# Optimization experiments

Hardware: AMD Instinct MI355X
Metric: run time of the kernel (lower is better)

Reference implementation:

```python
import jax, jax.numpy as jnp
import numpy as np

EMB = 768
N_HEADS = 12
HEAD_DIM = EMB // N_HEADS
EPS = 1e-5


def _gelu_tanh(x):
    c = jnp.sqrt(jnp.asarray(2.0 / jnp.pi, x.dtype))
    return 0.5 * x * (1.0 + jnp.tanh(c * (x + 0.044715 * x ** 3)))


def _layernorm(x, scale, shift):
    mean = jnp.mean(x, axis=-1, keepdims=True)
    var = jnp.mean((x - mean) ** 2, axis=-1, keepdims=True)
    return (x - mean) / jnp.sqrt(var + EPS) * scale + shift


def setup_inputs() -> dict:
    key = jax.random.key(0)
    ks = jax.random.split(key, 8)
    s = 0.02  # GPT-2 style init scale
    x = jax.random.normal(ks[0], (8, 1024, EMB), dtype=jnp.float32)
    # torch Linear weights are (out, in); no biases (qkv_bias=False everywhere)
    wq = jax.random.normal(ks[1], (EMB, EMB), dtype=jnp.float32) * s
    wk = jax.random.normal(ks[2], (EMB, EMB), dtype=jnp.float32) * s
    wv = jax.random.normal(ks[3], (EMB, EMB), dtype=jnp.float32) * s
    wo = jax.random.normal(ks[4], (EMB, EMB), dtype=jnp.float32) * s
    w1 = jax.random.normal(ks[5], (4 * EMB, EMB), dtype=jnp.float32) * s
    w2 = jax.random.normal(ks[6], (EMB, 4 * EMB), dtype=jnp.float32) * s
    ln1_scale = jnp.ones((EMB,), jnp.float32)
    ln1_shift = jnp.zeros((EMB,), jnp.float32)
    ln2_scale = jnp.ones((EMB,), jnp.float32)
    ln2_shift = jnp.zeros((EMB,), jnp.float32)
    return dict(x=x, wq=wq, wk=wk, wv=wv, wo=wo, w1=w1, w2=w2,
                ln1_scale=ln1_scale, ln1_shift=ln1_shift,
                ln2_scale=ln2_scale, ln2_shift=ln2_shift)


def reference(x, wq, wk, wv, wo, w1, w2, ln1_scale, ln1_shift, ln2_scale, ln2_shift):
    B, T, E = x.shape
    # --- attention sublayer (pre-LN) ---
    h = _layernorm(x, ln1_scale, ln1_shift)
    q = (h @ wq.T).reshape(B, T, N_HEADS, HEAD_DIM).transpose(0, 2, 1, 3)
    k = (h @ wk.T).reshape(B, T, N_HEADS, HEAD_DIM).transpose(0, 2, 1, 3)
    v = (h @ wv.T).reshape(B, T, N_HEADS, HEAD_DIM).transpose(0, 2, 1, 3)
    scores = jnp.einsum('bhqd,bhkd->bhqk', q, k)  # [B,H,T,T]
    causal = jnp.tril(jnp.ones((T, T), dtype=bool))
    scores = jnp.where(causal, scores, -jnp.inf)
    attn = jax.nn.softmax(scores / np.sqrt(HEAD_DIM), axis=-1)
    ctx = jnp.einsum('bhqk,bhkd->bhqd', attn, v)
    ctx = ctx.transpose(0, 2, 1, 3).reshape(B, T, E)
    x = x + ctx @ wo.T
    # --- FFN sublayer (pre-LN) ---
    h = _layernorm(x, ln2_scale, ln2_shift)
    h = _gelu_tanh(h @ w1.T) @ w2.T
    return x + h
```

## Files before the change

kernel.cpp:

```cpp
#include <hip/hip_runtime.h>
#include <hip/hip_bf16.h>
#include <cstdint>

#define EMB    768
#define NHEADS 12
#define HDIM   64
#define SEQ    1024
#define BATCH  8
#define MROWS  (BATCH*SEQ)
#define FFN    3072
#define W2E    (EMB*EMB)
#define W4E    (FFN*EMB)

typedef __bf16 bf16_t;
typedef bf16_t bf16x8 __attribute__((ext_vector_type(8)));
typedef float  f32x4  __attribute__((ext_vector_type(4)));

__device__ __forceinline__ float b2f(unsigned short u) {
    union { unsigned int i; float f; } t; t.i = ((unsigned int)u) << 16; return t.f;
}
__device__ __forceinline__ unsigned short f2b(float f) {
    union { float f; unsigned int i; } t; t.f = f;
    unsigned int lsb = (t.i >> 16) & 1u;
    t.i += 0x7fffu + lsb;
    return (unsigned short)(t.i >> 16);
}

#if defined(__has_builtin)
#if __has_builtin(__builtin_amdgcn_global_load_lds)
#define HAS_GLL 1
#endif
#endif
#ifndef HAS_GLL
#define HAS_GLL 0
#endif

__device__ __forceinline__ void gll16(const unsigned short* g, unsigned short* lds_wave_base) {
#if HAS_GLL
    __builtin_amdgcn_global_load_lds(
        (const __attribute__((address_space(1))) unsigned int*)g,
        (__attribute__((address_space(3))) unsigned int*)lds_wave_base, 16, 0, 0);
#endif
}

__device__ __forceinline__ int4 load8(const void* src, size_t eoff, bool f32) {
    if (f32) {
        const float4* p = reinterpret_cast<const float4*>((const float*)src + eoff);
        float4 a = p[0], b = p[1];
        union { unsigned short u[8]; int4 v; } r;
        r.u[0] = f2b(a.x); r.u[1] = f2b(a.y); r.u[2] = f2b(a.z); r.u[3] = f2b(a.w);
        r.u[4] = f2b(b.x); r.u[5] = f2b(b.y); r.u[6] = f2b(b.z); r.u[7] = f2b(b.w);
        return r.v;
    }
    return *reinterpret_cast<const int4*>((const unsigned short*)src + eoff);
}
__device__ __forceinline__ float4 load4f(const void* src, size_t eoff, bool f32) {
    if (f32) return *reinterpret_cast<const float4*>((const float*)src + eoff);
    ushort4 u = *reinterpret_cast<const ushort4*>((const unsigned short*)src + eoff);
    float4 r; r.x = b2f(u.x); r.y = b2f(u.y); r.z = b2f(u.z); r.w = b2f(u.w);
    return r;
}

struct DetectArgs { const unsigned short* p[11]; int n[11]; };

__global__ __launch_bounds__(256) void detect_all(DetectArgs a, int* __restrict__ flags) {
    __shared__ int cnt;
    if (threadIdx.x == 0) cnt = 0;
    __syncthreads();
    const unsigned short* src = a.p[blockIdx.x];
    int npairs = a.n[blockIdx.x] / 2;
    if (npairs > 4096) npairs = 4096;
    int local = 0;
    for (int p = threadIdx.x; p < npairs; p += 256) {
        unsigned short u0 = src[2 * p], u1 = src[2 * p + 1];
        int e0 = (u0 >> 7) & 0xFF;
        bool insane0 = (e0 == 0xFF) || (u0 != 0 && (e0 < 96 || e0 > 159));
        bool zpat    = (u0 == 0 && u1 != 0);
        if (insane0 || zpat) ++local;
    }
    atomicAdd(&cnt, local);
    __syncthreads();
    if (threadIdx.x == 0) flags[blockIdx.x] = (cnt * 8 > npairs) ? 1 : 0;
}

__global__ __launch_bounds__(256) void cvt_adapt(
        const void* __restrict__ src, unsigned short* __restrict__ dst,
        int n, const int* __restrict__ flag) {
    int i = blockIdx.x * 256 + threadIdx.x;
    if (i * 4 >= n) return;
    if (*flag) {
        float4 f = reinterpret_cast<const float4*>(src)[i];
        ushort4 o;
        o.x = f2b(f.x); o.y = f2b(f.y); o.z = f2b(f.z); o.w = f2b(f.w);
        reinterpret_cast<ushort4*>(dst)[i] = o;
    } else {
        reinterpret_cast<ushort4*>(dst)[i] = reinterpret_cast<const ushort4*>(src)[i];
    }
}

struct CvtArgs {
    const void* src[6];
    unsigned short* dst[6];
    int n[6];
    int blkoff[7];
    const int* F;
    int fidx[6];
};
__global__ __launch_bounds__(256) void cvt_weights(CvtArgs a) {
    int b = blockIdx.x, seg = 0;
    #pragma unroll
    for (int s = 0; s < 6; ++s) if (b >= a.blkoff[s + 1]) seg = s + 1;
    int i = (b - a.blkoff[seg]) * 256 + threadIdx.x;
    if (i * 4 >= a.n[seg]) return;
    if (a.F[a.fidx[seg]]) {
        float4 f = reinterpret_cast<const float4*>(a.src[seg])[i];
        ushort4 o;
        o.x = f2b(f.x); o.y = f2b(f.y); o.z = f2b(f.z); o.w = f2b(f.w);
        reinterpret_cast<ushort4*>(a.dst[seg])[i] = o;
    } else {
        reinterpret_cast<ushort4*>(a.dst[seg])[i] =
            reinterpret_cast<const ushort4*>(a.src[seg])[i];
    }
}

__global__ __launch_bounds__(256) void ln_kernel(
        const void* __restrict__ x,     const int* __restrict__ fx,
        const void* __restrict__ scale, const int* __restrict__ fsc,
        const void* __restrict__ shift, const int* __restrict__ fsh,
        unsigned short* __restrict__ out) {
    const bool xf = fx && *fx, scf = fsc && *fsc, shf = fsh && *fsh;
    int wave = threadIdx.x >> 6;
    int lane = threadIdx.x & 63;
    int row  = blockIdx.x * 4 + wave;
    const size_t rbase = (size_t)row * EMB;
    float v[12];
    float s = 0.f, s2 = 0.f;
    #pragma unroll
    for (int i = 0; i < 3; ++i) {
        float4 a = load4f(x, rbase + i * 256 + lane * 4, xf);
        v[i*4+0] = a.x; v[i*4+1] = a.y; v[i*4+2] = a.z; v[i*4+3] = a.w;
        s  += a.x + a.y + a.z + a.w;
        s2 += a.x*a.x + a.y*a.y + a.z*a.z + a.w*a.w;
    }
    #pragma unroll
    for (int off = 1; off < 64; off <<= 1) {
        s  += __shfl_xor(s,  off);
        s2 += __shfl_xor(s2, off);
    }
    float mean = s * (1.f / EMB);
    float var  = fmaxf(s2 * (1.f / EMB) - mean * mean, 0.f);
    float rstd = rsqrtf(var + 1e-5f);
    unsigned short* orow = out + rbase;
    #pragma unroll
    for (int i = 0; i < 3; ++i) {
        float4 sc = load4f(scale, i * 256 + lane * 4, scf);
        float4 sh = load4f(shift, i * 256 + lane * 4, shf);
        ushort4 o;
        o.x = f2b((v[i*4+0] - mean) * rstd * sc.x + sh.x);
        o.y = f2b((v[i*4+1] - mean) * rstd * sc.y + sh.y);
        o.z = f2b((v[i*4+2] - mean) * rstd * sc.z + sh.z);
        o.w = f2b((v[i*4+3] - mean) * rstd * sc.w + sh.w);
        *reinterpret_cast<ushort4*>(orow + i * 256 + lane * 4) = o;
    }
}

template<bool GELU, bool RESID, bool OUTF32>
__global__ __launch_bounds__(256) void gemm_lds(
        const unsigned short* __restrict__ A,
        const unsigned short* __restrict__ W,
        const void* R, const int* __restrict__ fR, size_t rOff,
        void* C, int M, int N, int K) {
    constexpr int BK = 32;
    __shared__ __align__(16) unsigned short sA[128 * BK];
    __shared__ __align__(16) unsigned short sB[128 * BK];
    const int m0 = blockIdx.x * 128, n0 = blockIdx.y * 128;
    const int t = threadIdx.x, wave = t >> 6, lane = t & 63;
    const int wrow = (wave >> 1) * 64, wcol = (wave & 1) * 64;
    const int quad = lane >> 4, lr = lane & 15;
    const int r0 = t >> 2;
    const int c0 = (t & 3) * 8;
    const bool rf = fR && *fR;

    f32x4 acc[4][4];
    #pragma unroll
    for (int i = 0; i < 4; ++i)
        #pragma unroll
        for (int j = 0; j < 4; ++j)
            acc[i][j] = (f32x4){0.f, 0.f, 0.f, 0.f};

    const unsigned short* gA0 = A + (size_t)(m0 + r0) * K + c0;
    const unsigned short* gA1 = A + (size_t)(m0 + 64 + r0) * K + c0;
    const unsigned short* gB0 = W + (size_t)(n0 + r0) * K + c0;
    const unsigned short* gB1 = W + (size_t)(n0 + 64 + r0) * K + c0;
    unsigned short* lA0 = sA + wave * 512;
    unsigned short* lA1 = sA + 2048 + wave * 512;
    unsigned short* lB0 = sB + wave * 512;
    unsigned short* lB1 = sB + 2048 + wave * 512;

    for (int k0 = 0; k0 < K; k0 += BK) {
#if HAS_GLL
        gll16(gA0 + k0, lA0);
        gll16(gA1 + k0, lA1);
        gll16(gB0 + k0, lB0);
        gll16(gB1 + k0, lB1);
#else
        *reinterpret_cast<int4*>(sA + t * 8)        = *reinterpret_cast<const int4*>(gA0 + k0);
        *reinterpret_cast<int4*>(sA + 2048 + t * 8) = *reinterpret_cast<const int4*>(gA1 + k0);
        *reinterpret_cast<int4*>(sB + t * 8)        = *reinterpret_cast<const int4*>(gB0 + k0);
        *reinterpret_cast<int4*>(sB + 2048 + t * 8) = *reinterpret_cast<const int4*>(gB1 + k0);
#endif
        __syncthreads();
        bf16x8 af[4], bfv[4];
        #pragma unroll
        for (int i = 0; i < 4; ++i)
            af[i] = *reinterpret_cast<const bf16x8*>(sA + (wrow + i * 16 + lr) * BK + quad * 8);
        #pragma unroll
        for (int j = 0; j < 4; ++j)
            bfv[j] = *reinterpret_cast<const bf16x8*>(sB + (wcol + j * 16 + lr) * BK + quad * 8);
        #pragma unroll
        for (int i = 0; i < 4; ++i)
            #pragma unroll
            for (int j = 0; j < 4; ++j)
                acc[i][j] = __builtin_amdgcn_mfma_f32_16x16x32_bf16(af[i], bfv[j], acc[i][j], 0, 0, 0);
        __syncthreads();
    }

    #pragma unroll
    for (int i = 0; i < 4; ++i) {
        #pragma unroll
        for (int j = 0; j < 4; ++j) {
            #pragma unroll
            for (int r = 0; r < 4; ++r) {
                int row = m0 + wrow + i * 16 + quad * 4 + r;
                int col = n0 + wcol + j * 16 + lr;
                float val = acc[i][j][r];
                if (GELU) {
                    float x3 = val * val * val;
                    val = 0.5f * val * (1.f + tanhf(0.7978845608028654f * (val + 0.044715f * x3)));
                }
                size_t idx = (size_t)row * N + col;
                if (RESID) {
                    float rv = rf ? ((const float*)R)[idx + rOff]
                                  : b2f(((const unsigned short*)R)[idx + rOff]);
                    val += rv;
                }
                if (OUTF32) ((float*)C)[idx] = val;
                else        ((unsigned short*)C)[idx] = f2b(val);
            }
        }
    }
}

template<bool GELU, bool RESID, bool OUTF32>
__global__ __launch_bounds__(256) void gemm_bt(
        const unsigned short* __restrict__ A,
        const void* __restrict__ W, const int* __restrict__ fW,
        const void* R, const int* __restrict__ fR, size_t rOff,
        void* C,
        int M, int N, int K) {
    const bool wf = fW && *fW;
    const bool rf = fR && *fR;
    constexpr int BK = 32, PAD = 8, LDW = BK + PAD;
    __shared__ __align__(16) unsigned short sA[128 * LDW];
    __shared__ __align__(16) unsigned short sB[128 * LDW];
    const int m0 = blockIdx.x * 128;
    const int n0 = blockIdx.y * 128;
    const int t    = threadIdx.x;
    const int wave = t >> 6, lane = t & 63;
    const int wrow = (wave >> 1) * 64, wcol = (wave & 1) * 64;
    const int quad = lane >> 4, lr = lane & 15;
    const int srow = t >> 2, scol = (t & 3) * 8;

    f32x4 acc[4][4];
    #pragma unroll
    for (int i = 0; i < 4; ++i)
        #pragma unroll
        for (int j = 0; j < 4; ++j)
            acc[i][j] = (f32x4){0.f, 0.f, 0.f, 0.f};

    const size_t aBase = (size_t)(m0 + srow) * K + scol;
    const size_t bBase = (size_t)(n0 + srow) * K + scol;

    for (int k0 = 0; k0 < K; k0 += BK) {
        int4 av0 = *reinterpret_cast<const int4*>(A + aBase + k0);
        int4 av1 = *reinterpret_cast<const int4*>(A + aBase + (size_t)64 * K + k0);
        int4 bv0 = load8(W, bBase + k0, wf);
        int4 bv1 = load8(W, bBase + (size_t)64 * K + k0, wf);
        *reinterpret_cast<int4*>(sA + srow * LDW + scol)        = av0;
        *reinterpret_cast<int4*>(sA + (srow + 64) * LDW + scol) = av1;
        *reinterpret_cast<int4*>(sB + srow * LDW + scol)        = bv0;
        *reinterpret_cast<int4*>(sB + (srow + 64) * LDW + scol) = bv1;
        __syncthreads();
        bf16x8 af[4], bfv[4];
        #pragma unroll
        for (int i = 0; i < 4; ++i)
            af[i] = *reinterpret_cast<const bf16x8*>(sA + (wrow + i * 16 + lr) * LDW + quad * 8);
        #pragma unroll
        for (int j = 0; j < 4; ++j)
            bfv[j] = *reinterpret_cast<const bf16x8*>(sB + (wcol + j * 16 + lr) * LDW + quad * 8);
        #pragma unroll
        for (int i = 0; i < 4; ++i)
            #pragma unroll
            for (int j = 0; j < 4; ++j)
                acc[i][j] = __builtin_amdgcn_mfma_f32_16x16x32_bf16(af[i], bfv[j], acc[i][j], 0, 0, 0);
        __syncthreads();
    }

    #pragma unroll
    for (int i = 0; i < 4; ++i) {
        #pragma unroll
        for (int j = 0; j < 4; ++j) {
            #pragma unroll
            for (int r = 0; r < 4; ++r) {
                int row = m0 + wrow + i * 16 + quad * 4 + r;
                int col = n0 + wcol + j * 16 + lr;
                float val = acc[i][j][r];
                if (GELU) {
                    float x3 = val * val * val;
                    val = 0.5f * val * (1.f + tanhf(0.7978845608028654f * (val + 0.044715f * x3)));
                }
                size_t idx = (size_t)row * N + col;
                if (RESID) {
                    float rv = rf ? ((const float*)R)[idx + rOff]
                                  : b2f(((const unsigned short*)R)[idx + rOff]);
                    val += rv;
                }
                if (OUTF32) ((float*)C)[idx] = val;
                else        ((unsigned short*)C)[idx] = f2b(val);
            }
        }
    }
}

__global__ __launch_bounds__(256) void fattn_kernel(
        const unsigned short* __restrict__ q,
        const unsigned short* __restrict__ k,
        const unsigned short* __restrict__ v,
        int rs, unsigned short* __restrict__ ctx) {
    constexpr int VTP = 72;
    __shared__ unsigned short Vt[64 * VTP];
    __shared__ unsigned short Pl[4][16 * VTP];
    const int tid  = threadIdx.x;
    const int wave = tid >> 6, lane = tid & 63;
    const int quad = lane >> 4, lr = lane & 15;
    const int NH   = gridDim.x >> 3;
    const int head = blockIdx.x % NH;
    const int pr   = blockIdx.x / NH;
    const int bb   = head / NHEADS, hd = head % NHEADS;
    const size_t seqbase = (size_t)bb * SEQ;

    #pragma unroll
    for (int seg = 0; seg < 2; ++seg) {
        const int qt = seg == 0 ? (15 - pr) : pr;
        const int q0 = qt * 64 + wave * 16;

        bf16x8 aQ0, aQ1;
        {
            const unsigned short* qp = q + (seqbase + q0 + lr) * rs + hd * HDIM + quad * 8;
            aQ0 = *reinterpret_cast<const bf16x8*>(qp);
            aQ1 = *reinterpret_cast<const bf16x8*>(qp + 32);
        }

        f32x4 O[4];
        #pragma unroll
        for (int i = 0; i < 4; ++i) O[i] = (f32x4){0.f, 0.f, 0.f, 0.f};
        float mrow[4], lrow[4];
        #pragma unroll
        for (int r = 0; r < 4; ++r) { mrow[r] = -__builtin_inff(); lrow[r] = 0.f; }

        for (int kt = 0; kt <= qt; ++kt) {
            {
                const int vrow = tid >> 2;
                const int vcol = (tid & 3) * 16;
                const unsigned short* vp = v + (seqbase + kt * 64 + vrow) * rs + hd * HDIM + vcol;
                union { int4 v4; unsigned short u[8]; } ua, ub;
                ua.v4 = *reinterpret_cast<const int4*>(vp);
                ub.v4 = *reinterpret_cast<const int4*>(vp + 8);
                #pragma unroll
                for (int e = 0; e < 8; ++e) Vt[(vcol + e) * VTP + vrow]     = ua.u[e];
                #pragma unroll
                for (int e = 0; e < 8; ++e) Vt[(vcol + 8 + e) * VTP + vrow] = ub.u[e];
            }
            __syncthreads();

            f32x4 S[4];
            #pragma unroll
            for (int sub = 0; sub < 4; ++sub) {
                const unsigned short* kp = k + (seqbase + kt * 64 + sub * 16 + lr) * rs + hd * HDIM + quad * 8;
                bf16x8 b0 = *reinterpret_cast<const bf16x8*>(kp);
                bf16x8 b1 = *reinterpret_cast<const bf16x8*>(kp + 32);
                f32x4 accS = (f32x4){0.f, 0.f, 0.f, 0.f};
                accS = __builtin_amdgcn_mfma_f32_16x16x32_bf16(aQ0, b0, accS, 0, 0, 0);
                accS = __builtin_amdgcn_mfma_f32_16x16x32_bf16(aQ1, b1, accS, 0, 0, 0);
                S[sub] = accS;
            }
            const bool diag = (kt == qt);
            #pragma unroll
            for (int sub = 0; sub < 4; ++sub) {
                const int kg = kt * 64 + sub * 16 + lr;
                #pragma unroll
                for (int r = 0; r < 4; ++r) {
                    float s = S[sub][r] * 0.125f;
                    if (diag && kg > q0 + quad * 4 + r) s = -__builtin_inff();
                    S[sub][r] = s;
                }
            }
            float mnew[4], alpha[4];
            #pragma unroll
            for (int r = 0; r < 4; ++r) {
                float mx = fmaxf(fmaxf(S[0][r], S[1][r]), fmaxf(S[2][r], S[3][r]));
                #pragma unroll
                for (int m = 1; m < 16; m <<= 1) mx = fmaxf(mx, __shfl_xor(mx, m));
                mnew[r]  = fmaxf(mrow[r], mx);
                alpha[r] = __expf(mrow[r] - mnew[r]);
                mrow[r]  = mnew[r];
            }
            float rsum[4] = {0.f, 0.f, 0.f, 0.f};
            #pragma unroll
            for (int sub = 0; sub < 4; ++sub)
                #pragma unroll
                for (int r = 0; r < 4; ++r) {
                    float p = __expf(S[sub][r] - mnew[r]);
                    S[sub][r] = p;
                    rsum[r] += p;
                }
            #pragma unroll
            for (int r = 0; r < 4; ++r) {
                float rs2 = rsum[r];
                #pragma unroll
                for (int m = 1; m < 16; m <<= 1) rs2 += __shfl_xor(rs2, m);
                lrow[r] = lrow[r] * alpha[r] + rs2;
            }
            #pragma unroll
            for (int d = 0; d < 4; ++d)
                #pragma unroll
                for (int r = 0; r < 4; ++r)
                    O[d][r] *= alpha[r];

            unsigned short* Pw = Pl[wave];
            #pragma unroll
            for (int sub = 0; sub < 4; ++sub)
                #pragma unroll
                for (int r = 0; r < 4; ++r)
                    Pw[(quad * 4 + r) * VTP + sub * 16 + lr] = f2b(S[sub][r]);
            __syncthreads();

            #pragma unroll
            for (int c = 0; c < 2; ++c) {
                bf16x8 aP = *reinterpret_cast<const bf16x8*>(&Pw[lr * VTP + c * 32 + quad * 8]);
                #pragma unroll
                for (int d = 0; d < 4; ++d) {
                    bf16x8 bV = *reinterpret_cast<const bf16x8*>(&Vt[(d * 16 + lr) * VTP + c * 32 + quad * 8]);
                    O[d] = __builtin_amdgcn_mfma_f32_16x16x32_bf16(aP, bV, O[d], 0, 0, 0);
                }
            }
            __syncthreads();
        }

        #pragma unroll
        for (int r = 0; r < 4; ++r) {
            const float rinv = 1.f / lrow[r];
            const int qg = q0 + quad * 4 + r;
            unsigned short* crow = ctx + (seqbase + qg) * EMB + hd * HDIM;
            #pragma unroll
            for (int d = 0; d < 4; ++d)
                crow[d * 16 + lr] = f2b(O[d][r] * rinv);
        }
    }
}

extern "C" void kernel_launch(void* const* d_in, const int* in_sizes, int n_in,
                              void* d_out, int out_size, void* d_ws, size_t ws_size,
                              hipStream_t stream) {
    const void* x  = d_in[0];
    const void* wq = d_in[1], *wk = d_in[2], *wv = d_in[3], *wo = d_in[4];
    const void* w1 = d_in[5], *w2 = d_in[6];
    const void* g1 = d_in[7], *s1 = d_in[8], *g2 = d_in[9], *s2 = d_in[10];
    char* ws = (char*)d_ws;
    dim3 blk(256);

    int* F = (int*)ws;
    {
        DetectArgs da;
        for (int i = 0; i < 11; ++i) { da.p[i] = (const unsigned short*)d_in[i]; da.n[i] = in_sizes[i]; }
        detect_all<<<11, blk, 0, stream>>>(da, F);
    }

    const size_t SZE = (size_t)MROWS * EMB;
    const size_t SZB = SZE * 2;
    unsigned short* base = (unsigned short*)(ws + 256);
    dim3 g768(MROWS / 128, EMB / 128);

    const size_t FULLB = 256 + 2ULL * (2 * W4E) + 2ULL * (4 * W2E)
                       + 2ULL * ((size_t)MROWS * 2304) + 2 * SZB
                       + 2ULL * ((size_t)MROWS * FFN);

    if (ws_size >= FULLB) {
        unsigned short* w1b   = base;
        unsigned short* w2b   = w1b + W4E;
        unsigned short* wqkvb = w2b + W4E;
        unsigned short* wob   = wqkvb + 3 * W2E;
        unsigned short* P     = wob + W2E;
        unsigned short* B0    = P + (size_t)MROWS * 2304;
        unsigned short* B1    = B0 + SZE;
        unsigned short* G     = B1 + SZE;

        {
            CvtArgs ca;
            ca.src[0] = wq; ca.src[1] = wk; ca.src[2] = wv;
            ca.src[3] = wo; ca.src[4] = w1; ca.src[5] = w2;
            ca.dst[0] = wqkvb; ca.dst[1] = wqkvb + W2E; ca.dst[2] = wqkvb + 2 * W2E;
            ca.dst[3] = wob;   ca.dst[4] = w1b;         ca.dst[5] = w2b;
            ca.n[0] = ca.n[1] = ca.n[2] = ca.n[3] = W2E; ca.n[4] = ca.n[5] = W4E;
            int off = 0;
            for (int s = 0; s < 6; ++s) { ca.blkoff[s] = off; off += ca.n[s] / 1024; }
            ca.blkoff[6] = off;
            ca.F = F;
            ca.fidx[0] = 1; ca.fidx[1] = 2; ca.fidx[2] = 3;
            ca.fidx[3] = 4; ca.fidx[4] = 5; ca.fidx[5] = 6;
            cvt_weights<<<off, blk, 0, stream>>>(ca);
        }

        ln_kernel<<<MROWS / 4, blk, 0, stream>>>(x, F+0, g1, F+7, s1, F+8, B1);
        dim3 gqkv(MROWS / 128, 2304 / 128);
        gemm_lds<false, false, false><<<gqkv, blk, 0, stream>>>(B1, wqkvb, nullptr, nullptr, 0, P, MROWS, 2304, EMB);
        fattn_kernel<<<BATCH * NHEADS * 8, blk, 0, stream>>>(P, P + 768, P + 1536, 2304, B0);
        gemm_lds<false, true, false><<<g768, blk, 0, stream>>>(B0, wob, x, F+0, 0, B1, MROWS, EMB, EMB);
        ln_kernel<<<MROWS / 4, blk, 0, stream>>>(B1, nullptr, g2, F+9, s2, F+10, B0);
        dim3 gffn1(MROWS / 128, FFN / 128);
        gemm_lds<true, false, false><<<gffn1, blk, 0, stream>>>(B0, w1b, nullptr, nullptr, 0, G, MROWS, FFN, EMB);
        gemm_lds<false, true, true><<<g768, blk, 0, stream>>>(G, w2b, B1, nullptr, 0, d_out, MROWS, EMB, FFN);
    } else if (ws_size >= 256 + 7 * SZB) {
        unsigned short* wqb = base;
        unsigned short* wkb = wqb + W2E;
        unsigned short* wvb = wkb + W2E;
        unsigned short* wob = wvb + W2E;
        unsigned short* w1b = wob + W2E;
        unsigned short* w2b = w1b + W4E;
        unsigned short* B0  = w2b + W4E;
        unsigned short* B1  = B0 + SZE;
        unsigned short* B2  = B1 + SZE;
        unsigned short* B3  = B2 + SZE;

        cvt_adapt<<<W2E / 1024, blk, 0, stream>>>(wq, wqb, W2E, F + 1);
        cvt_adapt<<<W2E / 1024, blk, 0, stream>>>(wk, wkb, W2E, F + 2);
        cvt_adapt<<<W2E / 1024, blk, 0, stream>>>(wv, wvb, W2E, F + 3);
        cvt_adapt<<<W2E / 1024, blk, 0, stream>>>(wo, wob, W2E, F + 4);
        cvt_adapt<<<W4E / 1024, blk, 0, stream>>>(w1, w1b, W4E, F + 5);
        cvt_adapt<<<W4E / 1024, blk, 0, stream>>>(w2, w2b, W4E, F + 6);

        ln_kernel<<<MROWS / 4, blk, 0, stream>>>(x, F+0, g1, F+7, s1, F+8, B0);
        gemm_lds<false, false, false><<<g768, blk, 0, stream>>>(B0, wqb, nullptr, nullptr, 0, B1, MROWS, EMB, EMB);
        gemm_lds<false, false, false><<<g768, blk, 0, stream>>>(B0, wkb, nullptr, nullptr, 0, B2, MROWS, EMB, EMB);
        gemm_lds<false, false, false><<<g768, blk, 0, stream>>>(B0, wvb, nullptr, nullptr, 0, B3, MROWS, EMB, EMB);
        fattn_kernel<<<BATCH * NHEADS * 8, blk, 0, stream>>>(B1, B2, B3, EMB, B0);
        gemm_lds<false, true, false><<<g768, blk, 0, stream>>>(B0, wob, x, F+0, 0, B1, MROWS, EMB, EMB);
        ln_kernel<<<MROWS / 4, blk, 0, stream>>>(B1, nullptr, g2, F+9, s2, F+10, B2);
        dim3 c3072(4096 / 128, FFN / 128), c768(4096 / 128, EMB / 128);
        for (int c = 0; c < 2; ++c) {
            const size_t r0 = (size_t)c * 4096;
            gemm_lds<true, false, false><<<c3072, blk, 0, stream>>>(B2 + r0 * EMB, w1b, nullptr, nullptr, 0, B3, 4096, FFN, EMB);
            gemm_lds<false, true, true><<<c768, blk, 0, stream>>>(B3, w2b, B1 + r0 * EMB, nullptr, 0, (float*)d_out + r0 * EMB, 4096, EMB, FFN);
        }
    } else if (ws_size >= 256 + 4 * SZB) {
        unsigned short* B0 = base;
        unsigned short* B1 = B0 + SZE;
        unsigned short* B2 = B1 + SZE;
        unsigned short* B3 = B2 + SZE;
        ln_kernel<<<MROWS / 4, blk, 0, stream>>>(x, F+0, g1, F+7, s1, F+8, B0);
        gemm_bt<false, false, false><<<g768, blk, 0, stream>>>(B0, wq, F+1, nullptr, nullptr, 0, B1, MROWS, EMB, EMB);
        gemm_bt<false, false, false><<<g768, blk, 0, stream>>>(B0, wk, F+2, nullptr, nullptr, 0, B2, MROWS, EMB, EMB);
        gemm_bt<false, false, false><<<g768, blk, 0, stream>>>(B0, wv, F+3, nullptr, nullptr, 0, B3, MROWS, EMB, EMB);
        fattn_kernel<<<BATCH * NHEADS * 8, blk, 0, stream>>>(B1, B2, B3, EMB, B0);
        gemm_bt<false, true, false><<<g768, blk, 0, stream>>>(B0, wo, F+4, x, F+0, 0, B1, MROWS, EMB, EMB);
        ln_kernel<<<MROWS / 4, blk, 0, stream>>>(B1, nullptr, g2, F+9, s2, F+10, B2);
        dim3 c3072(2048 / 128, FFN / 128), c768(2048 / 128, EMB / 128);
        for (int c = 0; c < 4; ++c) {
            const size_t r0 = (size_t)c * 2048;
            gemm_bt<true, false, false><<<c3072, blk, 0, stream>>>(B2 + r0 * EMB, w1, F+5, nullptr, nullptr, 0, B3, 2048, FFN, EMB);
            gemm_bt<false, true, true><<<c768, blk, 0, stream>>>(B3, w2, F+6, B1 + r0 * EMB, nullptr, 0, (float*)d_out + r0 * EMB, 2048, EMB, FFN);
        }
    } else {
        unsigned short* hlow = (unsigned short*)d_out;
        unsigned short* x2up = (unsigned short*)d_out + SZE;
        unsigned short* wsQ = base;
        unsigned short* wsK = wsQ + (size_t)1024 * EMB;
        unsigned short* wsV = wsK + (size_t)1024 * EMB;
        unsigned short* wsC = wsV + (size_t)1024 * EMB;
        ln_kernel<<<MROWS / 4, blk, 0, stream>>>(x, F+0, g1, F+7, s1, F+8, hlow);
        dim3 q768(1024 / 128, EMB / 128);
        for (int grp = 0; grp < BATCH; ++grp) {
            const size_t r0 = (size_t)grp * 1024;
            gemm_bt<false, false, false><<<q768, blk, 0, stream>>>(hlow + r0 * EMB, wq, F+1, nullptr, nullptr, 0, wsQ, 1024, EMB, EMB);
            gemm_bt<false, false, false><<<q768, blk, 0, stream>>>(hlow + r0 * EMB, wk, F+2, nullptr, nullptr, 0, wsK, 1024, EMB, EMB);
            gemm_bt<false, false, false><<<q768, blk, 0, stream>>>(hlow + r0 * EMB, wv, F+3, nullptr, nullptr, 0, wsV, 1024, EMB, EMB);
            fattn_kernel<<<1 * NHEADS * 8, blk, 0, stream>>>(wsQ, wsK, wsV, EMB, wsC);
            gemm_bt<false, true, false><<<q768, blk, 0, stream>>>(wsC, wo, F+4, x, F+0, r0 * EMB, x2up + r0 * EMB, 1024, EMB, EMB);
        }
        unsigned short* xb = base;
        unsigned short* h2 = xb + (size_t)1024 * EMB;
        unsigned short* gb = h2 + (size_t)1024 * EMB;
        dim3 f3072(1024 / 128, FFN / 128), f768(1024 / 128, EMB / 128);
        for (int c = 0; c < BATCH; ++c) {
            const size_t r0 = (size_t)c * 1024;
            hipMemcpyAsync(xb, x2up + r0 * EMB, (size_t)1024 * EMB * 2,
                           hipMemcpyDeviceToDevice, stream);
            ln_kernel<<<1024 / 4, blk, 0, stream>>>(xb, nullptr, g2, F+9, s2, F+10, h2);
            gemm_bt<true, false, false><<<f3072, blk, 0, stream>>>(h2, w1, F+5, nullptr, nullptr, 0, gb, 1024, FFN, EMB);
            gemm_bt<false, true, true><<<f768, blk, 0, stream>>>(gb, w2, F+6, xb, nullptr, 0, (float*)d_out + r0 * EMB, 1024, EMB, FFN);
        }
    }
}
```

Measured before the change: 451.2 us.

## Split-K the FFN down-projection GEMM with a separate reduce-plus-residual kernel

Adds a split-K path for the second FFN GEMM (K=3072). It launches twice the blocks, each covering half of K and writing fp32 partials to new workspace. A small kernel then sums the two partials with the bf16 residual into the output. This raises parallelism for the 384-block down-projection on a large-CU GPU, at the cost of extra fp32 partial traffic and an extra launch. The old 7-buffer fallback path is removed, and the previous full path is kept as a fallback when workspace is smaller.

```diff
diff --git a/kernel.cpp b/kernel.cpp
--- a/kernel.cpp
+++ b/kernel.cpp
@@ -123,6 +123,22 @@
     }
 }
 
+__global__ __launch_bounds__(256) void reduce2_kernel(
+        const float* __restrict__ P, const unsigned short* __restrict__ resid,
+        float* __restrict__ out, int n4) {
+    int i = blockIdx.x * 256 + threadIdx.x;
+    if (i >= n4) return;
+    float4 a = reinterpret_cast<const float4*>(P)[i];
+    float4 b = reinterpret_cast<const float4*>(P + (size_t)MROWS * EMB)[i];
+    ushort4 r = reinterpret_cast<const ushort4*>(resid)[i];
+    float4 o;
+    o.x = a.x + b.x + b2f(r.x);
+    o.y = a.y + b.y + b2f(r.y);
+    o.z = a.z + b.z + b2f(r.z);
+    o.w = a.w + b.w + b2f(r.w);
+    reinterpret_cast<float4*>(out)[i] = o;
+}
+
 __global__ __launch_bounds__(256) void ln_kernel(
         const void* __restrict__ x,     const int* __restrict__ fx,
         const void* __restrict__ scale, const int* __restrict__ fsc,
@@ -169,11 +185,12 @@
         const unsigned short* __restrict__ A,
         const unsigned short* __restrict__ W,
         const void* R, const int* __restrict__ fR, size_t rOff,
-        void* C, int M, int N, int K) {
+        void* C, int M, int N, int K, int lda, int ldw) {
     constexpr int BK = 32;
     __shared__ __align__(16) unsigned short sA[128 * BK];
     __shared__ __align__(16) unsigned short sB[128 * BK];
     const int m0 = blockIdx.x * 128, n0 = blockIdx.y * 128;
+    const int kz = blockIdx.z;
     const int t = threadIdx.x, wave = t >> 6, lane = t & 63;
     const int wrow = (wave >> 1) * 64, wcol = (wave & 1) * 64;
     const int quad = lane >> 4, lr = lane & 15;
@@ -181,6 +198,9 @@
     const int c0 = (t & 3) * 8;
     const bool rf = fR && *fR;
 
+    A += (size_t)kz * K;
+    W += (size_t)kz * K;
+
     f32x4 acc[4][4];
     #pragma unroll
     for (int i = 0; i < 4; ++i)
@@ -188,10 +208,10 @@
         for (int j = 0; j < 4; ++j)
             acc[i][j] = (f32x4){0.f, 0.f, 0.f, 0.f};
 
-    const unsigned short* gA0 = A + (size_t)(m0 + r0) * K + c0;
-    const unsigned short* gA1 = A + (size_t)(m0 + 64 + r0) * K + c0;
-    const unsigned short* gB0 = W + (size_t)(n0 + r0) * K + c0;
-    const unsigned short* gB1 = W + (size_t)(n0 + 64 + r0) * K + c0;
+    const unsigned short* gA0 = A + (size_t)(m0 + r0) * lda + c0;
+    const unsigned short* gA1 = A + (size_t)(m0 + 64 + r0) * lda + c0;
+    const unsigned short* gB0 = W + (size_t)(n0 + r0) * ldw + c0;
+    const unsigned short* gB1 = W + (size_t)(n0 + 64 + r0) * ldw + c0;
     unsigned short* lA0 = sA + wave * 512;
     unsigned short* lA1 = sA + 2048 + wave * 512;
     unsigned short* lB0 = sB + wave * 512;
@@ -225,6 +245,7 @@
         __syncthreads();
     }
 
+    float* Cf = (float*)C + (size_t)kz * M * N;
     #pragma unroll
     for (int i = 0; i < 4; ++i) {
         #pragma unroll
@@ -244,7 +265,7 @@
                                   : b2f(((const unsigned short*)R)[idx + rOff]);
                     val += rv;
                 }
-                if (OUTF32) ((float*)C)[idx] = val;
+                if (OUTF32) Cf[idx] = val;
                 else        ((unsigned short*)C)[idx] = f2b(val);
             }
         }
@@ -494,8 +515,9 @@
     const size_t FULLB = 256 + 2ULL * (2 * W4E) + 2ULL * (4 * W2E)
                        + 2ULL * ((size_t)MROWS * 2304) + 2 * SZB
                        + 2ULL * ((size_t)MROWS * FFN);
-
-    if (ws_size >= FULLB) {
+    const size_t FULLB2 = FULLB + 2ULL * SZE * 4;
+
+    if (ws_size >= FULLB2) {
         unsigned short* w1b   = base;
         unsigned short* w2b   = w1b + W4E;
         unsigned short* wqkvb = w2b + W4E;
@@ -504,6 +526,7 @@
         unsigned short* B0    = P + (size_t)MROWS * 2304;
         unsigned short* B1    = B0 + SZE;
         unsigned short* G     = B1 + SZE;
+        float*          PK    = (float*)(G + (size_t)MROWS * FFN);
 
         {
             CvtArgs ca;
@@ -523,45 +546,50 @@
 
         ln_kernel<<<MROWS / 4, blk, 0, stream>>>(x, F+0, g1, F+7, s1, F+8, B1);
         dim3 gqkv(MROWS / 128, 2304 / 128);
-        gemm_lds<false, false, false><<<gqkv, blk, 0, stream>>>(B1, wqkvb, nullptr, nullptr, 0, P, MROWS, 2304, EMB);
+        gemm_lds<false, false, false><<<gqkv, blk, 0, stream>>>(B1, wqkvb, nullptr, nullptr, 0, P, MROWS, 2304, EMB, EMB, EMB);
         fattn_kernel<<<BATCH * NHEADS * 8, blk, 0, stream>>>(P, P + 768, P + 1536, 2304, B0);
-        gemm_lds<false, true, false><<<g768, blk, 0, stream>>>(B0, wob, x, F+0, 0, B1, MROWS, EMB, EMB);
+        gemm_lds<false, true, false><<<g768, blk, 0, stream>>>(B0, wob, x, F+0, 0, B1, MROWS, EMB, EMB, EMB, EMB);
         ln_kernel<<<MROWS / 4, blk, 0, stream>>>(B1, nullptr, g2, F+9, s2, F+10, B0);
         dim3 gffn1(MROWS / 128, FFN / 128);
-        gemm_lds<true, false, false><<<gffn1, blk, 0, stream>>>(B0, w1b, nullptr, nullptr, 0, G, MROWS, FFN, EMB);
-        gemm_lds<false, true, true><<<g768, blk, 0, stream>>>(G, w2b, B1, nullptr, 0, d_out, MROWS, EMB, FFN);
-    } else if (ws_size >= 256 + 7 * SZB) {
-        unsigned short* wqb = base;
-        unsigned short* wkb = wqb + W2E;
-        unsigned short* wvb = wkb + W2E;
-        unsigned short* wob = wvb + W2E;
-        unsigned short* w1b = wob + W2E;
-        unsigned short* w2b = w1b + W4E;
-        unsigned short* B0  = w2b + W4E;
-        unsigned short* B1  = B0 + SZE;
-        unsigned short* B2  = B1 + SZE;
-        unsigned short* B3  = B2 + SZE;
-
-        cvt_adapt<<<W2E / 1024, blk, 0, stream>>>(wq, wqb, W2E, F + 1);
-        cvt_adapt<<<W2E / 1024, blk, 0, stream>>>(wk, wkb, W2E, F + 2);
-        cvt_adapt<<<W2E / 1024, blk, 0, stream>>>(wv, wvb, W2E, F + 3);
-        cvt_adapt<<<W2E / 1024, blk, 0, stream>>>(wo, wob, W2E, F + 4);
-        cvt_adapt<<<W4E / 1024, blk, 0, stream>>>(w1, w1b, W4E, F + 5);
-        cvt_adapt<<<W4E / 1024, blk, 0, stream>>>(w2, w2b, W4E, F + 6);
-
-        ln_kernel<<<MROWS / 4, blk, 0, stream>>>(x, F+0, g1, F+7, s1, F+8, B0);
-        gemm_lds<false, false, false><<<g768, blk, 0, stream>>>(B0, wqb, nullptr, nullptr, 0, B1, MROWS, EMB, EMB);
-        gemm_lds<false, false, false><<<g768, blk, 0, stream>>>(B0, wkb, nullptr, nullptr, 0, B2, MROWS, EMB, EMB);
-        gemm_lds<false, false, false><<<g768, blk, 0, stream>>>(B0, wvb, nullptr, nullptr, 0, B3, MROWS, EMB, EMB);
-        fattn_kernel<<<BATCH * NHEADS * 8, blk, 0, stream>>>(B1, B2, B3, EMB, B0);
-        gemm_lds<false, true, false><<<g768, blk, 0, stream>>>(B0, wob, x, F+0, 0, B1, MROWS, EMB, EMB);
-        ln_kernel<<<MROWS / 4, blk, 0, stream>>>(B1, nullptr, g2, F+9, s2, F+10, B2);
-        dim3 c3072(4096 / 128, FFN / 128), c768(4096 / 128, EMB / 128);
-        for (int c = 0; c < 2; ++c) {
-            const size_t r0 = (size_t)c * 4096;
-            gemm_lds<true, false, false><<<c3072, blk, 0, stream>>>(B2 + r0 * EMB, w1b, nullptr, nullptr, 0, B3, 4096, FFN, EMB);
-            gemm_lds<false, true, true><<<c768, blk, 0, stream>>>(B3, w2b, B1 + r0 * EMB, nullptr, 0, (float*)d_out + r0 * EMB, 4096, EMB, FFN);
-        }
+        gemm_lds<true, false, false><<<gffn1, blk, 0, stream>>>(B0, w1b, nullptr, nullptr, 0, G, MROWS, FFN, EMB, EMB, EMB);
+        dim3 gsk(MROWS / 128, EMB / 128, 2);
+        gemm_lds<false, false, true><<<gsk, blk, 0, stream>>>(G, w2b, nullptr, nullptr, 0, PK, MROWS, EMB, FFN / 2, FFN, FFN);
+        reduce2_kernel<<<(SZE / 4 + 255) / 256, blk, 0, stream>>>(PK, B1, (float*)d_out, SZE / 4);
+    } else if (ws_size >= FULLB) {
+        unsigned short* w1b   = base;
+        unsigned short* w2b   = w1b + W4E;
+        unsigned short* wqkvb = w2b + W4E;
+        unsigned short* wob   = wqkvb + 3 * W2E;
+        unsigned short* P     = wob + W2E;
+        unsigned short* B0    = P + (size_t)MROWS * 2304;
+        unsigned short* B1    = B0 + SZE;
+        unsigned short* G     = B1 + SZE;
+
+        {
+            CvtArgs ca;
+            ca.src[0] = wq; ca.src[1] = wk; ca.src[2] = wv;
+            ca.src[3] = wo; ca.src[4] = w1; ca.src[5] = w2;
+            ca.dst[0] = wqkvb; ca.dst[1] = wqkvb + W2E; ca.dst[2] = wqkvb + 2 * W2E;
+            ca.dst[3] = wob;   ca.dst[4] = w1b;         ca.dst[5] = w2b;
+            ca.n[0] = ca.n[1] = ca.n[2] = ca.n[3] = W2E; ca.n[4] = ca.n[5] = W4E;
+            int off = 0;
+            for (int s = 0; s < 6; ++s) { ca.blkoff[s] = off; off += ca.n[s] / 1024; }
+            ca.blkoff[6] = off;
+            ca.F = F;
+            ca.fidx[0] = 1; ca.fidx[1] = 2; ca.fidx[2] = 3;
+            ca.fidx[3] = 4; ca.fidx[4] = 5; ca.fidx[5] = 6;
+            cvt_weights<<<off, blk, 0, stream>>>(ca);
+        }
+
+        ln_kernel<<<MROWS / 4, blk, 0, stream>>>(x, F+0, g1, F+7, s1, F+8, B1);
+        dim3 gqkv(MROWS / 128, 2304 / 128);
+        gemm_lds<false, false, false><<<gqkv, blk, 0, stream>>>(B1, wqkvb, nullptr, nullptr, 0, P, MROWS, 2304, EMB, EMB, EMB);
+        fattn_kernel<<<BATCH * NHEADS * 8, blk, 0, stream>>>(P, P + 768, P + 1536, 2304, B0);
+        gemm_lds<false, true, false><<<g768, blk, 0, stream>>>(B0, wob, x, F+0, 0, B1, MROWS, EMB, EMB, EMB, EMB);
+        ln_kernel<<<MROWS / 4, blk, 0, stream>>>(B1, nullptr, g2, F+9, s2, F+10, B0);
+        dim3 gffn1(MROWS / 128, FFN / 128);
+        gemm_lds<true, false, false><<<gffn1, blk, 0, stream>>>(B0, w1b, nullptr, nullptr, 0, G, MROWS, FFN, EMB, EMB, EMB);
+        gemm_lds<false, true, true><<<g768, blk, 0, stream>>>(G, w2b, B1, nullptr, 0, d_out, MROWS, EMB, FFN, FFN, FFN);
     } else if (ws_size >= 256 + 4 * SZB) {
         unsigned short* B0 = base;
         unsigned short* B1 = B0 + SZE;
```

Result: faster. 440.2 us (-2.4%).
